# Performance work log

Hardware: AMD Instinct MI355X
Metric: run time of the kernel (lower is better)

Reference implementation:

```python
import jax, jax.numpy as jnp
import numpy as np
from jax import lax

# LeNet C3 sparse connectivity table: output map -> list of input channels
CONN = [
    [0, 1, 2], [1, 2, 3], [2, 3, 4], [3, 4, 5], [0, 4, 5], [0, 1, 5],          # 6 three-input maps
    [0, 1, 2, 3], [1, 2, 3, 4], [2, 3, 4, 5], [0, 3, 4, 5], [0, 1, 4, 5],      # 9 four-input maps
    [0, 1, 2, 5], [0, 1, 3, 4], [1, 2, 4, 5], [0, 2, 3, 5],
    [0, 1, 2, 3, 4, 5],                                                         # 1 six-input map
]

def _conn_mask():
    m = np.zeros((16, 6), dtype=np.float32)
    for o, chs in enumerate(CONN):
        m[o, chs] = 1.0
    return m[:, :, None, None]  # [O, I, 1, 1]


def setup_inputs() -> dict:
    key = jax.random.key(0)
    kx, kw, kb = jax.random.split(key, 3)
    x = jax.random.normal(kx, (2048, 6, 64, 64), dtype=jnp.float32)
    # fan-in-ish init; only masked entries ever contribute
    W = jax.random.normal(kw, (16, 6, 5, 5), dtype=jnp.float32) * 0.1
    b = jax.random.normal(kb, (16,), dtype=jnp.float32) * 0.01
    return {"x": x, "W": W, "b": b}


def reference(x, W, b):
    # The 16 tiny channel-gathered convs are mathematically a single dense
    # 6->16 VALID 5x5 conv whose weights are zero on non-connected channels.
    Wm = W * jnp.asarray(_conn_mask())                     # [16, 6, 5, 5]
    out = lax.conv_general_dilated(
        x, Wm, window_strides=(1, 1), padding="VALID",
        dimension_numbers=("NCHW", "OIHW", "NCHW"),
    )                                                      # [B, 16, 60, 60]
    return out + b[None, :, None, None]
```

## Files before the change

kernel.cpp:

```cpp
#include <hip/hip_runtime.h>

#define THREADS 384
#define RB 12
#define IN_ROWS 16
#define PS 64
#define LDS_FLOATS (6 * IN_ROWS * PS)

#define DECL(OC) float A0_##OC = bias[OC], A1_##OC = bias[OC]

#define LOADX(IC) do { \
    const float* p_ = brow + (IC) * (IN_ROWS * PS); \
    xa0 = p_[0];      xa1 = p_[1];      xa2 = p_[2];      xa3 = p_[3];      xa4 = p_[4]; \
    xb0 = p_[PS + 0]; xb1 = p_[PS + 1]; xb2 = p_[PS + 2]; xb3 = p_[PS + 3]; xb4 = p_[PS + 4]; \
} while (0)

#define UPD2(OC, IC) do { \
    const float* wp_ = Wky + (OC) * 150 + (IC) * 25; \
    const float w0_ = wp_[0], w1_ = wp_[1], w2_ = wp_[2], w3_ = wp_[3], w4_ = wp_[4]; \
    A0_##OC = fmaf(xa0, w0_, A0_##OC);  A1_##OC = fmaf(xb0, w0_, A1_##OC); \
    A0_##OC = fmaf(xa1, w1_, A0_##OC);  A1_##OC = fmaf(xb1, w1_, A1_##OC); \
    A0_##OC = fmaf(xa2, w2_, A0_##OC);  A1_##OC = fmaf(xb2, w2_, A1_##OC); \
    A0_##OC = fmaf(xa3, w3_, A0_##OC);  A1_##OC = fmaf(xb3, w3_, A1_##OC); \
    A0_##OC = fmaf(xa4, w4_, A0_##OC);  A1_##OC = fmaf(xb4, w4_, A1_##OC); \
} while (0)

#define SBAR __builtin_amdgcn_sched_barrier(0)

#define CHAN0 LOADX(0); UPD2(0,0);  UPD2(4,0);  UPD2(5,0);  UPD2(6,0);  UPD2(9,0);  UPD2(10,0); UPD2(11,0); UPD2(12,0); UPD2(14,0); UPD2(15,0); SBAR
#define CHAN1 LOADX(1); UPD2(0,1);  UPD2(1,1);  UPD2(5,1);  UPD2(6,1);  UPD2(7,1);  UPD2(10,1); UPD2(11,1); UPD2(12,1); UPD2(13,1); UPD2(15,1); SBAR
#define CHAN2 LOADX(2); UPD2(0,2);  UPD2(1,2);  UPD2(2,2);  UPD2(6,2);  UPD2(7,2);  UPD2(8,2);  UPD2(11,2); UPD2(13,2); UPD2(14,2); UPD2(15,2); SBAR
#define CHAN3 LOADX(3); UPD2(1,3);  UPD2(2,3);  UPD2(3,3);  UPD2(6,3);  UPD2(7,3);  UPD2(8,3);  UPD2(9,3);  UPD2(12,3); UPD2(14,3); UPD2(15,3); SBAR
#define CHAN4 LOADX(4); UPD2(2,4);  UPD2(3,4);  UPD2(4,4);  UPD2(7,4);  UPD2(8,4);  UPD2(9,4);  UPD2(10,4); UPD2(12,4); UPD2(13,4); UPD2(15,4); SBAR
#define CHAN5 LOADX(5); UPD2(3,5);  UPD2(4,5);  UPD2(5,5);  UPD2(8,5);  UPD2(9,5);  UPD2(10,5); UPD2(11,5); UPD2(13,5); UPD2(14,5); UPD2(15,5); SBAR

#define ST(T, OC) op[(OC) * 3600 + (T) * 60] = A##T##_##OC

__global__ __launch_bounds__(THREADS, 4)
void c3_conv(const float* __restrict__ x, const float* __restrict__ W,
             const float* __restrict__ bias, float* __restrict__ out) {
    __shared__ float xs[LDS_FLOATS + 4];

    const int blk  = blockIdx.x;
    const int img  = blk / 5;
    const int band = blk - img * 5;
    const int r0   = band * RB;
    const int t    = threadIdx.x;

    {
        const float4* src = reinterpret_cast<const float4*>(x) + (size_t)img * 6144;
        float4* dst = reinterpret_cast<float4*>(xs);
        #pragma unroll
        for (int k = 0; k < 4; ++k) {
            int s  = t + k * THREADS;
            int ic = s >> 8;
            int iy = (s >> 4) & 15;
            int c4 = s & 15;
            dst[s] = src[ic * 1024 + (r0 + iy) * 16 + c4];
        }
    }
    __syncthreads();

    const int w    = t >> 6;
    const int lr0  = 2 * w;
    const int lane = t & 63;

    DECL(0);  DECL(1);  DECL(2);  DECL(3);  DECL(4);  DECL(5);  DECL(6);  DECL(7);
    DECL(8);  DECL(9);  DECL(10); DECL(11); DECL(12); DECL(13); DECL(14); DECL(15);

    float xa0, xa1, xa2, xa3, xa4;
    float xb0, xb1, xb2, xb3, xb4;

    #pragma unroll 1
    for (int ky = 0; ky < 5; ++ky) {
        const float* brow = xs + (lr0 + ky) * PS + lane;
        const float* Wky  = W + ky * 5;
        CHAN0; CHAN1; CHAN2; CHAN3; CHAN4; CHAN5;
    }

    if (lane < 60) {
        float* op = out + (size_t)img * 57600 + (size_t)(r0 + lr0) * 60 + lane;
        ST(0,0);  ST(0,1);  ST(0,2);  ST(0,3);  ST(0,4);  ST(0,5);  ST(0,6);  ST(0,7);
        ST(0,8);  ST(0,9);  ST(0,10); ST(0,11); ST(0,12); ST(0,13); ST(0,14); ST(0,15);
        ST(1,0);  ST(1,1);  ST(1,2);  ST(1,3);  ST(1,4);  ST(1,5);  ST(1,6);  ST(1,7);
        ST(1,8);  ST(1,9);  ST(1,10); ST(1,11); ST(1,12); ST(1,13); ST(1,14); ST(1,15);
    }
}

extern "C" void kernel_launch(void* const* d_in, const int* in_sizes, int n_in,
                              void* d_out, int out_size, void* d_ws, size_t ws_size,
                              hipStream_t stream) {
    const float* x  = (const float*)d_in[0];
    const float* W  = (const float*)d_in[1];
    const float* b  = (const float*)d_in[2];
    float* out      = (float*)d_out;

    const int nimg = in_sizes[0] / (6 * 64 * 64);
    dim3 grid(nimg * 5), block(THREADS);
    hipLaunchKernelGGL(c3_conv, grid, block, 0, stream, x, W, b, out);
}
```

Before: 329.7 us.

## Compute four output rows per thread with 20-row bands per block

Each thread now accumulates four output rows instead of two for all 16 maps. Each block covers a 20-row band with 5 waves, so there are 3 blocks per image instead of 5. Weight loads (scalar or uniform) are amortized over twice as many FMAs, and the redundant halo rows loaded per image drop. The cost is register pressure from 64 accumulators plus 20 input values, which may lower occupancy or cause spills, and the larger LDS footprint lowers blocks per CU.

```diff
diff --git a/kernel.cpp b/kernel.cpp
--- a/kernel.cpp
+++ b/kernel.cpp
@@ -1,39 +1,48 @@
 #include <hip/hip_runtime.h>
 
-#define THREADS 384
-#define RB 12
-#define IN_ROWS 16
+#define THREADS 320
+#define RB 20
+#define IN_ROWS 24
 #define PS 64
 #define LDS_FLOATS (6 * IN_ROWS * PS)
 
-#define DECL(OC) float A0_##OC = bias[OC], A1_##OC = bias[OC]
+#define DECL(OC) float A0_##OC = bias[OC], A1_##OC = bias[OC], \
+                       A2_##OC = bias[OC], A3_##OC = bias[OC]
 
 #define LOADX(IC) do { \
     const float* p_ = brow + (IC) * (IN_ROWS * PS); \
-    xa0 = p_[0];      xa1 = p_[1];      xa2 = p_[2];      xa3 = p_[3];      xa4 = p_[4]; \
-    xb0 = p_[PS + 0]; xb1 = p_[PS + 1]; xb2 = p_[PS + 2]; xb3 = p_[PS + 3]; xb4 = p_[PS + 4]; \
+    xa0 = p_[0];        xa1 = p_[1];        xa2 = p_[2];        xa3 = p_[3];        xa4 = p_[4]; \
+    xb0 = p_[PS + 0];   xb1 = p_[PS + 1];   xb2 = p_[PS + 2];   xb3 = p_[PS + 3];   xb4 = p_[PS + 4]; \
+    xc0 = p_[2*PS + 0]; xc1 = p_[2*PS + 1]; xc2 = p_[2*PS + 2]; xc3 = p_[2*PS + 3]; xc4 = p_[2*PS + 4]; \
+    xd0 = p_[3*PS + 0]; xd1 = p_[3*PS + 1]; xd2 = p_[3*PS + 2]; xd3 = p_[3*PS + 3]; xd4 = p_[3*PS + 4]; \
 } while (0)
 
-#define UPD2(OC, IC) do { \
+#define UPD4(OC, IC) do { \
     const float* wp_ = Wky + (OC) * 150 + (IC) * 25; \
     const float w0_ = wp_[0], w1_ = wp_[1], w2_ = wp_[2], w3_ = wp_[3], w4_ = wp_[4]; \
     A0_##OC = fmaf(xa0, w0_, A0_##OC);  A1_##OC = fmaf(xb0, w0_, A1_##OC); \
+    A2_##OC = fmaf(xc0, w0_, A2_##OC);  A3_##OC = fmaf(xd0, w0_, A3_##OC); \
     A0_##OC = fmaf(xa1, w1_, A0_##OC);  A1_##OC = fmaf(xb1, w1_, A1_##OC); \
+    A2_##OC = fmaf(xc1, w1_, A2_##OC);  A3_##OC = fmaf(xd1, w1_, A3_##OC); \
     A0_##OC = fmaf(xa2, w2_, A0_##OC);  A1_##OC = fmaf(xb2, w2_, A1_##OC); \
+    A2_##OC = fmaf(xc2, w2_, A2_##OC);  A3_##OC = fmaf(xd2, w2_, A3_##OC); \
     A0_##OC = fmaf(xa3, w3_, A0_##OC);  A1_##OC = fmaf(xb3, w3_, A1_##OC); \
+    A2_##OC = fmaf(xc3, w3_, A2_##OC);  A3_##OC = fmaf(xd3, w3_, A3_##OC); \
     A0_##OC = fmaf(xa4, w4_, A0_##OC);  A1_##OC = fmaf(xb4, w4_, A1_##OC); \
+    A2_##OC = fmaf(xc4, w4_, A2_##OC);  A3_##OC = fmaf(xd4, w4_, A3_##OC); \
 } while (0)
 
 #define SBAR __builtin_amdgcn_sched_barrier(0)
 
-#define CHAN0 LOADX(0); UPD2(0,0);  UPD2(4,0);  UPD2(5,0);  UPD2(6,0);  UPD2(9,0);  UPD2(10,0); UPD2(11,0); UPD2(12,0); UPD2(14,0); UPD2(15,0); SBAR
-#define CHAN1 LOADX(1); UPD2(0,1);  UPD2(1,1);  UPD2(5,1);  UPD2(6,1);  UPD2(7,1);  UPD2(10,1); UPD2(11,1); UPD2(12,1); UPD2(13,1); UPD2(15,1); SBAR
-#define CHAN2 LOADX(2); UPD2(0,2);  UPD2(1,2);  UPD2(2,2);  UPD2(6,2);  UPD2(7,2);  UPD2(8,2);  UPD2(11,2); UPD2(13,2); UPD2(14,2); UPD2(15,2); SBAR
-#define CHAN3 LOADX(3); UPD2(1,3);  UPD2(2,3);  UPD2(3,3);  UPD2(6,3);  UPD2(7,3);  UPD2(8,3);  UPD2(9,3);  UPD2(12,3); UPD2(14,3); UPD2(15,3); SBAR
-#define CHAN4 LOADX(4); UPD2(2,4);  UPD2(3,4);  UPD2(4,4);  UPD2(7,4);  UPD2(8,4);  UPD2(9,4);  UPD2(10,4); UPD2(12,4); UPD2(13,4); UPD2(15,4); SBAR
-#define CHAN5 LOADX(5); UPD2(3,5);  UPD2(4,5);  UPD2(5,5);  UPD2(8,5);  UPD2(9,5);  UPD2(10,5); UPD2(11,5); UPD2(13,5); UPD2(14,5); UPD2(15,5); SBAR
+#define CHAN0 LOADX(0); UPD4(0,0);  UPD4(4,0);  UPD4(5,0);  UPD4(6,0);  UPD4(9,0);  UPD4(10,0); UPD4(11,0); UPD4(12,0); UPD4(14,0); UPD4(15,0); SBAR
+#define CHAN1 LOADX(1); UPD4(0,1);  UPD4(1,1);  UPD4(5,1);  UPD4(6,1);  UPD4(7,1);  UPD4(10,1); UPD4(11,1); UPD4(12,1); UPD4(13,1); UPD4(15,1); SBAR
+#define CHAN2 LOADX(2); UPD4(0,2);  UPD4(1,2);  UPD4(2,2);  UPD4(6,2);  UPD4(7,2);  UPD4(8,2);  UPD4(11,2); UPD4(13,2); UPD4(14,2); UPD4(15,2); SBAR
+#define CHAN3 LOADX(3); UPD4(1,3);  UPD4(2,3);  UPD4(3,3);  UPD4(6,3);  UPD4(7,3);  UPD4(8,3);  UPD4(9,3);  UPD4(12,3); UPD4(14,3); UPD4(15,3); SBAR
+#define CHAN4 LOADX(4); UPD4(2,4);  UPD4(3,4);  UPD4(4,4);  UPD4(7,4);  UPD4(8,4);  UPD4(9,4);  UPD4(10,4); UPD4(12,4); UPD4(13,4); UPD4(15,4); SBAR
+#define CHAN5 LOADX(5); UPD4(3,5);  UPD4(4,5);  UPD4(5,5);  UPD4(8,5);  UPD4(9,5);  UPD4(10,5); UPD4(11,5); UPD4(13,5); UPD4(14,5); UPD4(15,5); SBAR
 
 #define ST(T, OC) op[(OC) * 3600 + (T) * 60] = A##T##_##OC
+#define STOC(OC) ST(0,OC); ST(1,OC); ST(2,OC); ST(3,OC)
 
 __global__ __launch_bounds__(THREADS, 4)
 void c3_conv(const float* __restrict__ x, const float* __restrict__ W,
@@ -41,8 +50,8 @@
     __shared__ float xs[LDS_FLOATS + 4];
 
     const int blk  = blockIdx.x;
-    const int img  = blk / 5;
-    const int band = blk - img * 5;
+    const int img  = blk / 3;
+    const int band = blk - img * 3;
     const int r0   = band * RB;
     const int t    = threadIdx.x;
 
@@ -50,18 +59,21 @@
         const float4* src = reinterpret_cast<const float4*>(x) + (size_t)img * 6144;
         float4* dst = reinterpret_cast<float4*>(xs);
         #pragma unroll
-        for (int k = 0; k < 4; ++k) {
-            int s  = t + k * THREADS;
-            int ic = s >> 8;
-            int iy = (s >> 4) & 15;
-            int c4 = s & 15;
-            dst[s] = src[ic * 1024 + (r0 + iy) * 16 + c4];
+        for (int k = 0; k < 8; ++k) {
+            int s = t + k * THREADS;
+            if (s < 6 * IN_ROWS * 16) {
+                int ic  = s / (IN_ROWS * 16);
+                int rem = s - ic * (IN_ROWS * 16);
+                int iy  = rem >> 4;
+                int c4  = rem & 15;
+                dst[s] = src[ic * 1024 + (r0 + iy) * 16 + c4];
+            }
         }
     }
     __syncthreads();
 
     const int w    = t >> 6;
-    const int lr0  = 2 * w;
+    const int lr0  = 4 * w;
     const int lane = t & 63;
 
     DECL(0);  DECL(1);  DECL(2);  DECL(3);  DECL(4);  DECL(5);  DECL(6);  DECL(7);
@@ -69,6 +81,8 @@
 
     float xa0, xa1, xa2, xa3, xa4;
     float xb0, xb1, xb2, xb3, xb4;
+    float xc0, xc1, xc2, xc3, xc4;
+    float xd0, xd1, xd2, xd3, xd4;
 
     #pragma unroll 1
     for (int ky = 0; ky < 5; ++ky) {
@@ -79,10 +93,8 @@
 
     if (lane < 60) {
         float* op = out + (size_t)img * 57600 + (size_t)(r0 + lr0) * 60 + lane;
-        ST(0,0);  ST(0,1);  ST(0,2);  ST(0,3);  ST(0,4);  ST(0,5);  ST(0,6);  ST(0,7);
-        ST(0,8);  ST(0,9);  ST(0,10); ST(0,11); ST(0,12); ST(0,13); ST(0,14); ST(0,15);
-        ST(1,0);  ST(1,1);  ST(1,2);  ST(1,3);  ST(1,4);  ST(1,5);  ST(1,6);  ST(1,7);
-        ST(1,8);  ST(1,9);  ST(1,10); ST(1,11); ST(1,12); ST(1,13); ST(1,14); ST(1,15);
+        STOC(0);  STOC(1);  STOC(2);  STOC(3);  STOC(4);  STOC(5);  STOC(6);  STOC(7);
+        STOC(8);  STOC(9);  STOC(10); STOC(11); STOC(12); STOC(13); STOC(14); STOC(15);
     }
 }
 
@@ -95,6 +107,6 @@
     float* out      = (float*)d_out;
 
     const int nimg = in_sizes[0] / (6 * 64 * 64);
-    dim3 grid(nimg * 5), block(THREADS);
+    dim3 grid(nimg * 3), block(THREADS);
     hipLaunchKernelGGL(c3_conv, grid, block, 0, stream, x, W, b, out);
 }
```

New measurement: 683.2 us. 2.07x slower.
